# Optimization experiments

Measured on AMD Instinct MI355X. Metric: run time of the kernel, lower is better.

## Reference

```python
import jax, jax.numpy as jnp
import numpy as np

N_NODES = 50000
N_EDGES = 800000
D = 64  # node_dim == edge_dim
NEG_SLOPE = 0.2
EPS = 1e-5


def _lin_params(key, d_in, d_out):
    k1, k2 = jax.random.split(key)
    bound = 1.0 / np.sqrt(d_in)
    W = jax.random.uniform(k1, (d_out, d_in), minval=-bound, maxval=bound, dtype=jnp.float32)
    b = jax.random.uniform(k2, (d_out,), minval=-bound, maxval=bound, dtype=jnp.float32)
    return W, b


def setup_inputs() -> dict:
    key = jax.random.key(0)
    ks = jax.random.split(key, 12)
    V = jax.random.normal(ks[0], (N_NODES, D), dtype=jnp.float32)
    E = jax.random.normal(ks[1], (N_EDGES, D), dtype=jnp.float32)
    src = jax.random.randint(ks[2], (N_EDGES,), 0, N_NODES, dtype=jnp.int32)
    dst = jax.random.randint(ks[3], (N_EDGES,), 0, N_NODES, dtype=jnp.int32)
    pA_w, pA_b = _lin_params(ks[4], D, D)   # NodePooling.A
    pB_w, pB_b = _lin_params(ks[5], D, D)   # NodePooling.B
    mW1, mb1 = _lin_params(ks[6], D, D)     # edge MLP layer 1
    mW2, mb2 = _lin_params(ks[7], D, D)     # edge MLP layer 2
    BW, Bb = _lin_params(ks[8], D, D)       # GenMessage.B (scale)
    CW, Cb = _lin_params(ks[9], D, D)       # GenMessage.C (shift)
    return {"V": V, "E": E, "src": src, "dst": dst,
            "pA_w": pA_w, "pA_b": pA_b, "pB_w": pB_w, "pB_b": pB_b,
            "mW1": mW1, "mb1": mb1, "mW2": mW2, "mb2": mb2,
            "BW": BW, "Bb": Bb, "CW": CW, "Cb": Cb}


def _lrelu(x):
    return jnp.where(x >= 0, x, NEG_SLOPE * x)


def reference(V, E, src, dst, pA_w, pA_b, pB_w, pB_b, mW1, mb1, mW2, mb2, BW, Bb, CW, Cb):
    n = V.shape[0]
    # V = act(V); NodePooling: B(lrelu(A(V)))
    Va = _lrelu(V)
    Vp = _lrelu(Va @ pA_w.T + pA_b) @ pB_w.T + pB_b  # [N, D]
    # edge MLP on edge features (2 Linear+ReLU layers)
    x = jax.nn.relu(E @ mW1.T + mb1)
    x = jax.nn.relu(x @ mW2.T + mb2)                  # [E, D]
    scale = jax.nn.sigmoid(x @ BW.T + Bb)
    shift = x @ CW.T + Cb
    # gathered src features, gated affine message
    M1 = scale * Vp[src] + shift                      # [E, D]
    M2 = M1 * M1
    # segment-mean onto dst (DGL fn.mean); zero for isolated nodes
    deg = jax.ops.segment_sum(jnp.ones((dst.shape[0],), jnp.float32), dst, num_segments=n)
    denom = jnp.maximum(deg, 1.0)[:, None]
    V1 = jax.ops.segment_sum(M1, dst, num_segments=n) / denom
    V2 = jax.ops.segment_sum(M2, dst, num_segments=n) / denom
    return jnp.sqrt(jax.nn.relu(V2 - V1) + EPS)
```

## Files before the change

### kernel.cpp

```cpp
#include <hip/hip_runtime.h>

#define NN 50000
#define NE 800000
#define DDIM 64
#define PADX 68
#define PADK 72
#define PADM 69
#define NB_SCAN ((NN + 255) / 256)
#define NEG_SLOPE 0.2f
#define EPS_V 1e-5f

typedef short bf16x8 __attribute__((ext_vector_type(8)));
typedef float f32x4 __attribute__((ext_vector_type(4)));

__device__ __forceinline__ float lrelu_f(float x) { return x >= 0.0f ? x : NEG_SLOPE * x; }

__device__ __forceinline__ unsigned short bf16_rn(float x) {
    union { float f; unsigned int u; } c; c.f = x;
    unsigned int r = c.u + 0x7FFF + ((c.u >> 16) & 1);
    return (unsigned short)(r >> 16);
}
__device__ __forceinline__ float bf16_tof(unsigned short h) {
    union { float f; unsigned int u; } c; c.u = ((unsigned int)h) << 16;
    return c.f;
}

__device__ __forceinline__ void mma_tile(float acc[16], const float* __restrict__ XT,
                                         const float* __restrict__ Wc, int e0, int f0)
{
    #pragma unroll 4
    for (int kk = 0; kk < DDIM; kk += 4) {
        float4 A0 = *(const float4*)&XT[(kk+0)*PADX + e0];
        float4 A1 = *(const float4*)&XT[(kk+1)*PADX + e0];
        float4 A2 = *(const float4*)&XT[(kk+2)*PADX + e0];
        float4 A3 = *(const float4*)&XT[(kk+3)*PADX + e0];
        float4 B0 = *(const float4*)&Wc[(f0+0)*PADX + kk];
        float4 B1 = *(const float4*)&Wc[(f0+1)*PADX + kk];
        float4 B2 = *(const float4*)&Wc[(f0+2)*PADX + kk];
        float4 B3 = *(const float4*)&Wc[(f0+3)*PADX + kk];
        const float a[4][4] = {{A0.x,A0.y,A0.z,A0.w},{A1.x,A1.y,A1.z,A1.w},
                               {A2.x,A2.y,A2.z,A2.w},{A3.x,A3.y,A3.z,A3.w}};
        const float b[4][4] = {{B0.x,B0.y,B0.z,B0.w},{B1.x,B1.y,B1.z,B1.w},
                               {B2.x,B2.y,B2.z,B2.w},{B3.x,B3.y,B3.z,B3.w}};
        #pragma unroll
        for (int j = 0; j < 4; ++j)
            #pragma unroll
            for (int i = 0; i < 4; ++i)
                #pragma unroll
                for (int q = 0; q < 4; ++q)
                    acc[i*4+j] = fmaf(a[q][i], b[j][q], acc[i*4+j]);
    }
}

__device__ __forceinline__ void load_w_f32(float* __restrict__ Wc, const float* __restrict__ Wg, int tid)
{
    #pragma unroll
    for (int c = 0; c < 4; ++c) {
        int idx = (c << 10) + (tid << 2);
        int f = idx >> 6, k = idx & 63;
        *(float4*)&Wc[f*PADX + k] = *(const float4*)&Wg[idx];
    }
}

__global__ __launch_bounds__(256, 3)
void node_pool_kernel(const float* __restrict__ V,
                      const float* __restrict__ Aw, const float* __restrict__ Ab,
                      const float* __restrict__ Bw, const float* __restrict__ Bbv,
                      float* __restrict__ Vp,
                      const int* __restrict__ dst, int* __restrict__ degi)
{
    __shared__ float Wc[DDIM*PADX];
    __shared__ float XT[DDIM*PADX];
    const int tid = threadIdx.x;
    const int nb = blockIdx.x * 64;
    const int e0 = (tid & 15) << 2;
    const int f0 = (tid >> 4) << 2;

    #pragma unroll
    for (int c = 0; c < 4; ++c) {
        int idx = (c << 10) + (tid << 2);
        int e = idx >> 6, d = idx & 63;
        int row = nb + e; if (row > NN-1) row = NN-1;
        float4 v = *(const float4*)&V[(size_t)row*DDIM + d];
        XT[(d+0)*PADX + e] = lrelu_f(v.x);
        XT[(d+1)*PADX + e] = lrelu_f(v.y);
        XT[(d+2)*PADX + e] = lrelu_f(v.z);
        XT[(d+3)*PADX + e] = lrelu_f(v.w);
    }
    load_w_f32(Wc, Aw, tid);
    __syncthreads();

    float acc[16];
    #pragma unroll
    for (int i = 0; i < 16; ++i) acc[i] = 0.f;
    mma_tile(acc, XT, Wc, e0, f0);
    __syncthreads();

    {
        float4 bv = *(const float4*)&Ab[f0];
        const float ba[4] = {bv.x, bv.y, bv.z, bv.w};
        #pragma unroll
        for (int j = 0; j < 4; ++j) {
            float4 v;
            v.x = lrelu_f(acc[0*4+j] + ba[j]);
            v.y = lrelu_f(acc[1*4+j] + ba[j]);
            v.z = lrelu_f(acc[2*4+j] + ba[j]);
            v.w = lrelu_f(acc[3*4+j] + ba[j]);
            *(float4*)&XT[(f0+j)*PADX + e0] = v;
        }
    }
    load_w_f32(Wc, Bw, tid);
    __syncthreads();

    float acc2[16];
    #pragma unroll
    for (int i = 0; i < 16; ++i) acc2[i] = 0.f;
    mma_tile(acc2, XT, Wc, e0, f0);

    float4 bv = *(const float4*)&Bbv[f0];
    #pragma unroll
    for (int i = 0; i < 4; ++i) {
        int row = nb + e0 + i;
        if (row < NN) {
            float4 o;
            o.x = acc2[i*4+0] + bv.x;
            o.y = acc2[i*4+1] + bv.y;
            o.z = acc2[i*4+2] + bv.z;
            o.w = acc2[i*4+3] + bv.w;
            *(float4*)&Vp[(size_t)row*DDIM + f0] = o;
        }
    }

    const int stride = gridDim.x * 256;
    for (int e = blockIdx.x * 256 + tid; e < NE; e += stride)
        atomicAdd(&degi[dst[e]], 1);
}

__global__ __launch_bounds__(256)
void prep_w_kernel(const float* __restrict__ W1, const float* __restrict__ W2,
                   const float* __restrict__ WB, const float* __restrict__ WC,
                   short* __restrict__ WF)
{
    int gid = blockIdx.x * 256 + threadIdx.x;
    int L = gid >> 12, r = gid & 4095;
    int t = r >> 10, ks = (r >> 9) & 1, lane = (r >> 3) & 63, j = r & 7;
    const float* Ws = (L == 0) ? W1 : (L == 1) ? W2 : (L == 2) ? WB : WC;
    int n = lane & 15, kg = lane >> 4;
    int f = t*16 + n, k = ks*32 + kg*8 + j;
    float v = Ws[f*64 + k];
    unsigned short h = bf16_rn(v);
    unsigned short l = bf16_rn(v - bf16_tof(h));
    int base = L*8192 + ((t*2 + ks)*2)*512 + lane*8 + j;
    WF[base]       = (short)h;
    WF[base + 512] = (short)l;
}

__global__ __launch_bounds__(256)
void scan1_kernel(const int* __restrict__ degi, int* __restrict__ linc, int* __restrict__ bsum)
{
    __shared__ int ws[4];
    const int tid = threadIdx.x;
    const int lane = tid & 63, wv = tid >> 6;
    int i = blockIdx.x * 256 + tid;
    int v = (i < NN) ? degi[i] : 0;
    int sc = v;
    #pragma unroll
    for (int off = 1; off < 64; off <<= 1) {
        int t = __shfl_up(sc, off, 64);
        if (lane >= off) sc += t;
    }
    if (lane == 63) ws[wv] = sc;
    __syncthreads();
    int wb = 0;
    #pragma unroll
    for (int w = 0; w < 4; ++w) if (w < wv) wb += ws[w];
    int incl = sc + wb;
    if (i < NN) linc[i] = incl;
    if (tid == 255) bsum[blockIdx.x] = incl;
}

__global__ __launch_bounds__(256)
void scan23_kernel(const int* __restrict__ degi, const int* __restrict__ linc,
                   const int* __restrict__ bsum, int* __restrict__ curs)
{
    __shared__ int ws[4];
    __shared__ int base_s;
    const int tid = threadIdx.x;
    const int lane = tid & 63, wv = tid >> 6;
    int v = (tid < NB_SCAN) ? bsum[tid] : 0;
    int sc = v;
    #pragma unroll
    for (int off = 1; off < 64; off <<= 1) {
        int t = __shfl_up(sc, off, 64);
        if (lane >= off) sc += t;
    }
    if (lane == 63) ws[wv] = sc;
    __syncthreads();
    int wb = 0;
    #pragma unroll
    for (int w = 0; w < 4; ++w) if (w < wv) wb += ws[w];
    if (tid == blockIdx.x) base_s = sc + wb - v;
    __syncthreads();
    int i = blockIdx.x * 256 + tid;
    if (i < NN) curs[i] = base_s + linc[i] - degi[i];
}

__global__ __launch_bounds__(256)
void scatter_kernel(const int* __restrict__ dst, int* __restrict__ cursor, int* __restrict__ eidx)
{
    int e = blockIdx.x * 256 + threadIdx.x;
    if (e < NE) {
        int p = atomicAdd(&cursor[dst[e]], 1);
        eidx[p] = e;
    }
}

struct WFrags { bf16x8 bh[4][2]; bf16x8 bl[4][2]; };

__device__ __forceinline__ void load_wfrags(const short* __restrict__ WL, int lane, WFrags& w)
{
    #pragma unroll
    for (int t = 0; t < 4; ++t)
        #pragma unroll
        for (int ks = 0; ks < 2; ++ks) {
            w.bh[t][ks] = *(const bf16x8*)&WL[(((t*2 + ks)*2 + 0)*64 + lane)*8];
            w.bl[t][ks] = *(const bf16x8*)&WL[(((t*2 + ks)*2 + 1)*64 + lane)*8];
        }
}

__device__ __forceinline__ void mfma_gemm_r(const short* __restrict__ Xh, const short* __restrict__ Xl,
                                            const WFrags& w, int wv, int lane, f32x4 acc[4])
{
    const int m = lane & 15, kg = lane >> 4;
    const int arow = (wv*16 + m)*PADK + kg*8;
    bf16x8 ah0 = *(const bf16x8*)&Xh[arow];
    bf16x8 al0 = *(const bf16x8*)&Xl[arow];
    bf16x8 ah1 = *(const bf16x8*)&Xh[arow + 32];
    bf16x8 al1 = *(const bf16x8*)&Xl[arow + 32];
    #pragma unroll
    for (int t = 0; t < 4; ++t) {
        acc[t] = __builtin_amdgcn_mfma_f32_16x16x32_bf16(al0, w.bh[t][0], acc[t], 0, 0, 0);
        acc[t] = __builtin_amdgcn_mfma_f32_16x16x32_bf16(ah0, w.bl[t][0], acc[t], 0, 0, 0);
        acc[t] = __builtin_amdgcn_mfma_f32_16x16x32_bf16(ah0, w.bh[t][0], acc[t], 0, 0, 0);
        acc[t] = __builtin_amdgcn_mfma_f32_16x16x32_bf16(al1, w.bh[t][1], acc[t], 0, 0, 0);
        acc[t] = __builtin_amdgcn_mfma_f32_16x16x32_bf16(ah1, w.bl[t][1], acc[t], 0, 0, 0);
        acc[t] = __builtin_amdgcn_mfma_f32_16x16x32_bf16(ah1, w.bh[t][1], acc[t], 0, 0, 0);
    }
}

__device__ __forceinline__ void repack_relu(short* __restrict__ Xh, short* __restrict__ Xl,
                                            const f32x4 acc[4], const float* __restrict__ bias,
                                            int wv, int lane)
{
    const int n = lane & 15, mg = lane >> 4;
    #pragma unroll
    for (int t = 0; t < 4; ++t) {
        float b = bias[t*16 + n];
        #pragma unroll
        for (int r = 0; r < 4; ++r) {
            float y = fmaxf(acc[t][r] + b, 0.0f);
            int e = wv*16 + mg*4 + r;
            unsigned short h = bf16_rn(y);
            float lof = y - bf16_tof(h);
            Xh[e*PADK + t*16 + n] = (short)h;
            Xl[e*PADK + t*16 + n] = (short)bf16_rn(lof);
        }
    }
}

__global__ __launch_bounds__(256, 3)
void edge_kernel(const float* __restrict__ Eg,
                 const int* __restrict__ src, const int* __restrict__ dst,
                 const int* __restrict__ eidx,
                 const short* __restrict__ WF,
                 const float* __restrict__ b1, const float* __restrict__ b2,
                 const float* __restrict__ bB, const float* __restrict__ bC,
                 const float* __restrict__ Vp,
                 float* __restrict__ S1, float* __restrict__ S2)
{
    __shared__ __align__(16) char smem[2 * 64 * PADK * 2];
    __shared__ int srcs[64], dsts[64];
    short* Xh = (short*)smem;
    short* Xl = Xh + 64*PADK;
    float* M1T = (float*)smem;

    const int tid = threadIdx.x;
    const int lane = tid & 63, wv = tid >> 6;
    const int eb = blockIdx.x * 64;

    #pragma unroll
    for (int c = 0; c < 4; ++c) {
        int idx = (c << 10) + (tid << 2);
        int e = idx >> 6, d = idx & 63;
        int eg = eidx[eb + e];
        float4 v = *(const float4*)&Eg[(size_t)eg*DDIM + d];
        ushort4 h, l;
        h.x = bf16_rn(v.x); l.x = bf16_rn(v.x - bf16_tof(h.x));
        h.y = bf16_rn(v.y); l.y = bf16_rn(v.y - bf16_tof(h.y));
        h.z = bf16_rn(v.z); l.z = bf16_rn(v.z - bf16_tof(h.z));
        h.w = bf16_rn(v.w); l.w = bf16_rn(v.w - bf16_tof(h.w));
        *(ushort4*)&Xh[e*PADK + d] = h;
        *(ushort4*)&Xl[e*PADK + d] = l;
    }
    if (tid < 64) {
        int eg = eidx[eb + tid];
        srcs[tid] = src[eg];
        dsts[tid] = dst[eg];
    }
    WFrags w;
    load_wfrags(WF, lane, w);
    __syncthreads();

    f32x4 acc[4];
    #pragma unroll
    for (int t = 0; t < 4; ++t) acc[t] = (f32x4){0.f, 0.f, 0.f, 0.f};
    mfma_gemm_r(Xh, Xl, w, wv, lane, acc);
    __syncthreads();
    repack_relu(Xh, Xl, acc, b1, wv, lane);
    load_wfrags(WF + 8192, lane, w);
    __syncthreads();

    #pragma unroll
    for (int t = 0; t < 4; ++t) acc[t] = (f32x4){0.f, 0.f, 0.f, 0.f};
    mfma_gemm_r(Xh, Xl, w, wv, lane, acc);
    __syncthreads();
    repack_relu(Xh, Xl, acc, b2, wv, lane);
    load_wfrags(WF + 2*8192, lane, w);
    __syncthreads();

    f32x4 accS[4], accH[4];
    #pragma unroll
    for (int t = 0; t < 4; ++t) { accS[t] = (f32x4){0.f,0.f,0.f,0.f}; accH[t] = (f32x4){0.f,0.f,0.f,0.f}; }
    mfma_gemm_r(Xh, Xl, w, wv, lane, accS);
    load_wfrags(WF + 3*8192, lane, w);
    mfma_gemm_r(Xh, Xl, w, wv, lane, accH);
    __syncthreads();

    {
        const int n = lane & 15, mg = lane >> 4;
        int sn[4];
        #pragma unroll
        for (int r = 0; r < 4; ++r) sn[r] = srcs[wv*16 + mg*4 + r];
        #pragma unroll
        for (int t = 0; t < 4; ++t) {
            const int f = t*16 + n;
            const float bBv = bB[f];
            const float bCv = bC[f];
            #pragma unroll
            for (int r = 0; r < 4; ++r) {
                float vp = Vp[(size_t)sn[r]*DDIM + f];
                float sg = 1.0f / (1.0f + __expf(-(accS[t][r] + bBv)));
                float m1 = fmaf(sg, vp, accH[t][r] + bCv);
                M1T[f*PADM + wv*16 + mg*4 + r] = m1;
            }
        }
    }
    __syncthreads();

    const int f = tid >> 2;
    const int g = (tid & 3) << 4;
    float s1 = 0.f, s2 = 0.f;
    int prev = dsts[g];
    #pragma unroll 4
    for (int i = 0; i < 16; ++i) {
        int dn = dsts[g + i];
        float m1 = M1T[f*PADM + g + i];
        float m2 = m1 * m1;
        if (dn != prev) {
            atomicAdd(&S1[(size_t)prev*DDIM + f], s1);
            atomicAdd(&S2[(size_t)prev*DDIM + f], s2);
            s1 = 0.f; s2 = 0.f; prev = dn;
        }
        s1 += m1; s2 += m2;
    }
    atomicAdd(&S1[(size_t)prev*DDIM + f], s1);
    atomicAdd(&S2[(size_t)prev*DDIM + f], s2);
}

__global__ __launch_bounds__(256)
void finalize_kernel(const float* __restrict__ S1, const float* __restrict__ S2,
                     const int* __restrict__ degi, float* __restrict__ out)
{
    int gid = blockIdx.x * blockDim.x + threadIdx.x;
    if (gid >= NN*DDIM) return;
    int n = gid >> 6;
    float dn = (float)degi[n];
    dn = dn > 1.0f ? dn : 1.0f;
    float v = (S2[gid] - S1[gid]) / dn;
    out[gid] = sqrtf(fmaxf(v, 0.0f) + EPS_V);
}

extern "C" void kernel_launch(void* const* d_in, const int* in_sizes, int n_in,
                              void* d_out, int out_size, void* d_ws, size_t ws_size,
                              hipStream_t stream) {
    const float* V   = (const float*)d_in[0];
    const float* Eg  = (const float*)d_in[1];
    const int*   src = (const int*)d_in[2];
    const int*   dst = (const int*)d_in[3];
    const float* pAw = (const float*)d_in[4];
    const float* pAb = (const float*)d_in[5];
    const float* pBw = (const float*)d_in[6];
    const float* pBb = (const float*)d_in[7];
    const float* mW1 = (const float*)d_in[8];
    const float* mb1 = (const float*)d_in[9];
    const float* mW2 = (const float*)d_in[10];
    const float* mb2 = (const float*)d_in[11];
    const float* BW  = (const float*)d_in[12];
    const float* Bb  = (const float*)d_in[13];
    const float* CW  = (const float*)d_in[14];
    const float* Cb  = (const float*)d_in[15];
    float* out = (float*)d_out;

    float* ws    = (float*)d_ws;
    float* Vp    = ws;
    float* S1    = ws + (size_t)NN*DDIM;
    float* S2    = ws + (size_t)2*NN*DDIM;
    int*   degi  = (int*)(ws + (size_t)3*NN*DDIM);
    int*   curs  = degi + NN;
    int*   linc  = curs + NN;
    int*   bsum  = linc + NN;
    int*   bbase = bsum + NB_SCAN;
    int*   eidx  = bbase + NB_SCAN;
    short* WF    = (short*)(eidx + NE);

    hipMemsetAsync(S1, 0, (size_t)(2*NN*DDIM + NN) * sizeof(float), stream);

    prep_w_kernel<<<64, 256, 0, stream>>>(mW1, mW2, BW, CW, WF);
    node_pool_kernel<<<(NN + 63)/64, 256, 0, stream>>>(V, pAw, pAb, pBw, pBb, Vp, dst, degi);
    scan1_kernel<<<NB_SCAN, 256, 0, stream>>>(degi, linc, bsum);
    scan23_kernel<<<NB_SCAN, 256, 0, stream>>>(degi, linc, bsum, curs);
    scatter_kernel<<<(NE + 255)/256, 256, 0, stream>>>(dst, curs, eidx);
    edge_kernel<<<NE/64, 256, 0, stream>>>(Eg, src, dst, eidx, WF,
                                           mb1, mb2, Bb, Cb, Vp, S1, S2);
    finalize_kernel<<<(NN*DDIM + 255)/256, 256, 0, stream>>>(S1, S2, degi, out);
}
```

Baseline: 584.4 us.

## Make edge kernel wave-independent with per-wave LDS scratch and streamed weights

Restructures the edge MLP kernel so each wavefront handles its own 16 edges end to end. Inputs are loaded straight into MFMA A-fragments, and layer outputs are passed between layers through a small per-wave LDS transpose, with wave barriers instead of block-wide __syncthreads. Weight fragments are streamed per k-step rather than held in registers, which lowers register pressure and allows occupancy to rise to 4 blocks. The price is repeated global/L2 weight loads for every GEMM and more scattered per-lane Eg loads. The atomic segment reduction now runs over 16 edges per wave instead of 64 per block, which may mean more atomics.

```diff
diff --git a/kernel.cpp b/kernel.cpp
--- a/kernel.cpp
+++ b/kernel.cpp
@@ -4,8 +4,7 @@
 #define NE 800000
 #define DDIM 64
 #define PADX 68
-#define PADK 72
-#define PADM 69
+#define PADS 68
 #define NB_SCAN ((NN + 255) / 256)
 #define NEG_SLOPE 0.2f
 #define EPS_V 1e-5f
@@ -23,6 +22,16 @@
 __device__ __forceinline__ float bf16_tof(unsigned short h) {
     union { float f; unsigned int u; } c; c.u = ((unsigned int)h) << 16;
     return c.f;
+}
+
+__device__ __forceinline__ void split8(const float* __restrict__ v, bf16x8& h, bf16x8& l)
+{
+    #pragma unroll
+    for (int j = 0; j < 8; ++j) {
+        unsigned short hh = bf16_rn(v[j]);
+        h[j] = (short)hh;
+        l[j] = (short)bf16_rn(v[j] - bf16_tof(hh));
+    }
 }
 
 __device__ __forceinline__ void mma_tile(float acc[16], const float* __restrict__ XT,
@@ -215,60 +224,48 @@
     }
 }
 
-struct WFrags { bf16x8 bh[4][2]; bf16x8 bl[4][2]; };
-
-__device__ __forceinline__ void load_wfrags(const short* __restrict__ WL, int lane, WFrags& w)
-{
+__device__ __forceinline__ void gemm64(const short* __restrict__ WL, int lane,
+                                       const bf16x8 ah[2], const bf16x8 al[2], f32x4 acc[4])
+{
+    #pragma unroll
+    for (int ks = 0; ks < 2; ++ks) {
+        bf16x8 bh[4], bl[4];
+        #pragma unroll
+        for (int t = 0; t < 4; ++t) {
+            bh[t] = *(const bf16x8*)&WL[(((t*2 + ks)*2 + 0)*64 + lane)*8];
+            bl[t] = *(const bf16x8*)&WL[(((t*2 + ks)*2 + 1)*64 + lane)*8];
+        }
+        #pragma unroll
+        for (int t = 0; t < 4; ++t) {
+            acc[t] = __builtin_amdgcn_mfma_f32_16x16x32_bf16(al[ks], bh[t], acc[t], 0, 0, 0);
+            acc[t] = __builtin_amdgcn_mfma_f32_16x16x32_bf16(ah[ks], bl[t], acc[t], 0, 0, 0);
+            acc[t] = __builtin_amdgcn_mfma_f32_16x16x32_bf16(ah[ks], bh[t], acc[t], 0, 0, 0);
+        }
+    }
+}
+
+__device__ __forceinline__ void transpose_frags(float* __restrict__ sw, const f32x4 y[4],
+                                                int lane, bf16x8 ah[2], bf16x8 al[2])
+{
+    const int n = lane & 15, mg = lane >> 4;
     #pragma unroll
     for (int t = 0; t < 4; ++t)
         #pragma unroll
-        for (int ks = 0; ks < 2; ++ks) {
-            w.bh[t][ks] = *(const bf16x8*)&WL[(((t*2 + ks)*2 + 0)*64 + lane)*8];
-            w.bl[t][ks] = *(const bf16x8*)&WL[(((t*2 + ks)*2 + 1)*64 + lane)*8];
-        }
-}
-
-__device__ __forceinline__ void mfma_gemm_r(const short* __restrict__ Xh, const short* __restrict__ Xl,
-                                            const WFrags& w, int wv, int lane, f32x4 acc[4])
-{
+        for (int r = 0; r < 4; ++r)
+            sw[(mg*4 + r)*PADS + t*16 + n] = y[t][r];
+    __builtin_amdgcn_wave_barrier();
     const int m = lane & 15, kg = lane >> 4;
-    const int arow = (wv*16 + m)*PADK + kg*8;
-    bf16x8 ah0 = *(const bf16x8*)&Xh[arow];
-    bf16x8 al0 = *(const bf16x8*)&Xl[arow];
-    bf16x8 ah1 = *(const bf16x8*)&Xh[arow + 32];
-    bf16x8 al1 = *(const bf16x8*)&Xl[arow + 32];
-    #pragma unroll
-    for (int t = 0; t < 4; ++t) {
-        acc[t] = __builtin_amdgcn_mfma_f32_16x16x32_bf16(al0, w.bh[t][0], acc[t], 0, 0, 0);
-        acc[t] = __builtin_amdgcn_mfma_f32_16x16x32_bf16(ah0, w.bl[t][0], acc[t], 0, 0, 0);
-        acc[t] = __builtin_amdgcn_mfma_f32_16x16x32_bf16(ah0, w.bh[t][0], acc[t], 0, 0, 0);
-        acc[t] = __builtin_amdgcn_mfma_f32_16x16x32_bf16(al1, w.bh[t][1], acc[t], 0, 0, 0);
-        acc[t] = __builtin_amdgcn_mfma_f32_16x16x32_bf16(ah1, w.bl[t][1], acc[t], 0, 0, 0);
-        acc[t] = __builtin_amdgcn_mfma_f32_16x16x32_bf16(ah1, w.bh[t][1], acc[t], 0, 0, 0);
-    }
-}
-
-__device__ __forceinline__ void repack_relu(short* __restrict__ Xh, short* __restrict__ Xl,
-                                            const f32x4 acc[4], const float* __restrict__ bias,
-                                            int wv, int lane)
-{
-    const int n = lane & 15, mg = lane >> 4;
-    #pragma unroll
-    for (int t = 0; t < 4; ++t) {
-        float b = bias[t*16 + n];
-        #pragma unroll
-        for (int r = 0; r < 4; ++r) {
-            float y = fmaxf(acc[t][r] + b, 0.0f);
-            int e = wv*16 + mg*4 + r;
-            unsigned short h = bf16_rn(y);
-            float lof = y - bf16_tof(h);
-            Xh[e*PADK + t*16 + n] = (short)h;
-            Xl[e*PADK + t*16 + n] = (short)bf16_rn(lof);
-        }
-    }
-}
-
-__global__ __launch_bounds__(256, 3)
+    float x[16];
+    *(float4*)&x[0]  = *(const float4*)&sw[m*PADS + kg*8];
+    *(float4*)&x[4]  = *(const float4*)&sw[m*PADS + kg*8 + 4];
+    *(float4*)&x[8]  = *(const float4*)&sw[m*PADS + 32 + kg*8];
+    *(float4*)&x[12] = *(const float4*)&sw[m*PADS + 32 + kg*8 + 4];
+    split8(&x[0], ah[0], al[0]);
+    split8(&x[8], ah[1], al[1]);
+    __builtin_amdgcn_wave_barrier();
+}
+
+__global__ __launch_bounds__(256, 4)
 void edge_kernel(const float* __restrict__ Eg,
                  const int* __restrict__ src, const int* __restrict__ dst,
                  const int* __restrict__ eidx,
@@ -278,69 +275,69 @@
                  const float* __restrict__ Vp,
                  float* __restrict__ S1, float* __restrict__ S2)
 {
-    __shared__ __align__(16) char smem[2 * 64 * PADK * 2];
-    __shared__ int srcs[64], dsts[64];
-    short* Xh = (short*)smem;
-    short* Xl = Xh + 64*PADK;
-    float* M1T = (float*)smem;
+    __shared__ float scratch[4 * 16 * PADS];
+    __shared__ int aux[4 * 32];
 
     const int tid = threadIdx.x;
     const int lane = tid & 63, wv = tid >> 6;
-    const int eb = blockIdx.x * 64;
-
-    #pragma unroll
-    for (int c = 0; c < 4; ++c) {
-        int idx = (c << 10) + (tid << 2);
-        int e = idx >> 6, d = idx & 63;
-        int eg = eidx[eb + e];
-        float4 v = *(const float4*)&Eg[(size_t)eg*DDIM + d];
-        ushort4 h, l;
-        h.x = bf16_rn(v.x); l.x = bf16_rn(v.x - bf16_tof(h.x));
-        h.y = bf16_rn(v.y); l.y = bf16_rn(v.y - bf16_tof(h.y));
-        h.z = bf16_rn(v.z); l.z = bf16_rn(v.z - bf16_tof(h.z));
-        h.w = bf16_rn(v.w); l.w = bf16_rn(v.w - bf16_tof(h.w));
-        *(ushort4*)&Xh[e*PADK + d] = h;
-        *(ushort4*)&Xl[e*PADK + d] = l;
-    }
-    if (tid < 64) {
-        int eg = eidx[eb + tid];
-        srcs[tid] = src[eg];
-        dsts[tid] = dst[eg];
-    }
-    WFrags w;
-    load_wfrags(WF, lane, w);
-    __syncthreads();
+    float* sw = scratch + wv * 16 * PADS;
+    int* auxw = aux + wv * 32;
+
+    const int ew = blockIdx.x * 64 + wv * 16;
+    const int m = lane & 15, kg = lane >> 4;
+
+    int eg = eidx[ew + m];
+    if (lane < 16) {
+        auxw[lane]      = src[eg];
+        auxw[16 + lane] = dst[eg];
+    }
+    bf16x8 ah[2], al[2];
+    {
+        const float* er = Eg + (size_t)eg*DDIM + kg*8;
+        float x[16];
+        *(float4*)&x[0]  = *(const float4*)&er[0];
+        *(float4*)&x[4]  = *(const float4*)&er[4];
+        *(float4*)&x[8]  = *(const float4*)&er[32];
+        *(float4*)&x[12] = *(const float4*)&er[36];
+        split8(&x[0], ah[0], al[0]);
+        split8(&x[8], ah[1], al[1]);
+    }
+
+    const int n = lane & 15, mg = lane >> 4;
 
     f32x4 acc[4];
     #pragma unroll
     for (int t = 0; t < 4; ++t) acc[t] = (f32x4){0.f, 0.f, 0.f, 0.f};
-    mfma_gemm_r(Xh, Xl, w, wv, lane, acc);
-    __syncthreads();
-    repack_relu(Xh, Xl, acc, b1, wv, lane);
-    load_wfrags(WF + 8192, lane, w);
-    __syncthreads();
+    gemm64(WF, lane, ah, al, acc);
+    #pragma unroll
+    for (int t = 0; t < 4; ++t) {
+        float b = b1[t*16 + n];
+        #pragma unroll
+        for (int r = 0; r < 4; ++r) acc[t][r] = fmaxf(acc[t][r] + b, 0.0f);
+    }
+    transpose_frags(sw, acc, lane, ah, al);
 
     #pragma unroll
     for (int t = 0; t < 4; ++t) acc[t] = (f32x4){0.f, 0.f, 0.f, 0.f};
-    mfma_gemm_r(Xh, Xl, w, wv, lane, acc);
-    __syncthreads();
-    repack_relu(Xh, Xl, acc, b2, wv, lane);
-    load_wfrags(WF + 2*8192, lane, w);
-    __syncthreads();
+    gemm64(WF + 8192, lane, ah, al, acc);
+    #pragma unroll
+    for (int t = 0; t < 4; ++t) {
+        float b = b2[t*16 + n];
+        #pragma unroll
+        for (int r = 0; r < 4; ++r) acc[t][r] = fmaxf(acc[t][r] + b, 0.0f);
+    }
+    transpose_frags(sw, acc, lane, ah, al);
 
     f32x4 accS[4], accH[4];
     #pragma unroll
     for (int t = 0; t < 4; ++t) { accS[t] = (f32x4){0.f,0.f,0.f,0.f}; accH[t] = (f32x4){0.f,0.f,0.f,0.f}; }
-    mfma_gemm_r(Xh, Xl, w, wv, lane, accS);
-    load_wfrags(WF + 3*8192, lane, w);
-    mfma_gemm_r(Xh, Xl, w, wv, lane, accH);
-    __syncthreads();
+    gemm64(WF + 2*8192, lane, ah, al, accS);
+    gemm64(WF + 3*8192, lane, ah, al, accH);
 
     {
-        const int n = lane & 15, mg = lane >> 4;
         int sn[4];
         #pragma unroll
-        for (int r = 0; r < 4; ++r) sn[r] = srcs[wv*16 + mg*4 + r];
+        for (int r = 0; r < 4; ++r) sn[r] = auxw[mg*4 + r];
         #pragma unroll
         for (int t = 0; t < 4; ++t) {
             const int f = t*16 + n;
@@ -351,20 +348,19 @@
                 float vp = Vp[(size_t)sn[r]*DDIM + f];
                 float sg = 1.0f / (1.0f + __expf(-(accS[t][r] + bBv)));
                 float m1 = fmaf(sg, vp, accH[t][r] + bCv);
-                M1T[f*PADM + wv*16 + mg*4 + r] = m1;
+                sw[(mg*4 + r)*PADS + f] = m1;
             }
         }
     }
-    __syncthreads();
-
-    const int f = tid >> 2;
-    const int g = (tid & 3) << 4;
+    __builtin_amdgcn_wave_barrier();
+
+    const int f = lane;
     float s1 = 0.f, s2 = 0.f;
-    int prev = dsts[g];
+    int prev = auxw[16];
     #pragma unroll 4
-    for (int i = 0; i < 16; ++i) {
-        int dn = dsts[g + i];
-        float m1 = M1T[f*PADM + g + i];
+    for (int e = 0; e < 16; ++e) {
+        int dn = auxw[16 + e];
+        float m1 = sw[e*PADS + f];
         float m2 = m1 * m1;
         if (dn != prev) {
             atomicAdd(&S1[(size_t)prev*DDIM + f], s1);
```

Measured after the change: 581.5 us. About the same (-0.5%).
